# Performance work log

Hardware: AMD Instinct MI355X
Metric: run time of the kernel (lower is better)

## Reference

```python
import jax, jax.numpy as jnp
import numpy as np

HIDDEN = 2048
NUM_EXPERTS = 64
TOP_K = 8
EPS = 1e-6


def setup_inputs() -> dict:
    key = jax.random.key(0)
    k1, k2, k3, k4 = jax.random.split(key, 4)
    hidden_states = jax.random.normal(k1, (4, 4096, HIDDEN), dtype=jnp.float32)
    scale = jnp.ones((HIDDEN,), dtype=jnp.float32) + 0.01 * jax.random.normal(k2, (HIDDEN,), dtype=jnp.float32)
    proj_w = jax.random.normal(k3, (NUM_EXPERTS, HIDDEN), dtype=jnp.float32) * (HIDDEN ** -0.5)
    per_expert_scale = jnp.ones((NUM_EXPERTS,), dtype=jnp.float32) + 0.01 * jax.random.normal(k4, (NUM_EXPERTS,), dtype=jnp.float32)
    return {"hidden_states": hidden_states, "scale": scale, "proj_w": proj_w, "per_expert_scale": per_expert_scale}


def reference(hidden_states, scale, proj_w, per_expert_scale):
    H = hidden_states.shape[-1]
    # RMSNorm without learned scale
    x = hidden_states * jax.lax.rsqrt(jnp.mean(hidden_states * hidden_states, axis=-1, keepdims=True) + EPS)
    # elementwise scale and 1/sqrt(H) root-size scaling
    x = x * scale * (H ** -0.5)
    # router logits: [B,S,E]
    logits = jnp.einsum("bsh,eh->bse", x, proj_w)
    router_probs = jax.nn.softmax(logits.astype(jnp.float32), axis=-1)
    top_k_weights, top_k_index = jax.lax.top_k(router_probs, TOP_K)
    top_k_weights = top_k_weights / jnp.sum(top_k_weights, axis=-1, keepdims=True)
    top_k_weights = top_k_weights * per_expert_scale[top_k_index]
    # histc with bins=E, min=0, max=E on integer indices == bincount
    num_tokens_per_expert = jnp.bincount(top_k_index.reshape(-1), length=NUM_EXPERTS).astype(jnp.float32)
    return (top_k_weights.astype(hidden_states.dtype), top_k_index, num_tokens_per_expert)
```

## Files before the change

### kernel.cpp

```cpp
#include <hip/hip_runtime.h>
#include <math.h>

#define HIDDEN   2048
#define NEXPERT  64
#define TOPK     8
#define NTOK     16384
#define TOKB     16
#define RSQRT_H  0.02209708691207961
#define WSCALE   64.0f

typedef __attribute__((ext_vector_type(8))) _Float16       v8h;
typedef __attribute__((ext_vector_type(8))) unsigned short v8u;
typedef __attribute__((ext_vector_type(4))) float          v4f;

static __device__ __forceinline__ unsigned short f16b(float x) {
    return __builtin_bit_cast(unsigned short, (_Float16)x);
}
static __device__ __forceinline__ float f16f(unsigned short u) {
    return (float)__builtin_bit_cast(_Float16, u);
}

__global__ __launch_bounds__(256) void prep_wf(
    const float* __restrict__ w, const float* __restrict__ scale,
    unsigned short* __restrict__ wf, float* __restrict__ out_c)
{
    int i    = blockIdx.x * 256 + threadIdx.x;
    if (i < NEXPERT) out_c[i] = 0.f;
    int j    = i & 7;
    int lane = (i >> 3) & 63;
    int nt   = (i >> 9) & 3;
    int ks   = i >> 11;
    int e    = nt * 16 + (lane & 15);
    int k    = ks * 32 + (lane >> 4) * 8 + j;
    float v  = w[e * HIDDEN + k] * scale[k] * WSCALE;
    unsigned short vh = f16b(v);
    unsigned short vl = f16b(v - f16f(vh));
    size_t base = (((size_t)(ks * 4 + nt) * 2) * 64 + lane) * 8 + j;
    wf[base]       = vh;
    wf[base + 512] = vl;
}

__global__ __launch_bounds__(512, 8) void router_main(
    const float* __restrict__ h, const unsigned short* __restrict__ wf,
    const float* __restrict__ pes,
    float* __restrict__ out_w, float* __restrict__ out_i, float* __restrict__ out_c)
{
    __shared__ __align__(16) float lg[8 * 16 * 65];
    __shared__ float lss[8 * 16];
    __shared__ int   hist[NEXPERT];

    const int tid  = (int)threadIdx.x;
    const int w    = __builtin_amdgcn_readfirstlane(tid >> 6);
    const int lane = tid & 63;
    const int m    = lane & 15;
    const int quad = lane >> 4;
    const int t0   = (int)blockIdx.x * TOKB;

    if (tid < NEXPERT) hist[tid] = 0;

    const float* xp = h + (size_t)(t0 + m) * HIDDEN + w * 256 + quad * 8;
    const unsigned short* wq = wf + (size_t)(w * 8) * 4096 + (size_t)lane * 8;

    v4f acc[4];
#pragma unroll
    for (int nt = 0; nt < 4; ++nt) acc[nt] = (v4f)0.f;
    float ssl = 0.f;

    float4 xa = *(const float4*)xp;
    float4 xb = *(const float4*)(xp + 4);

    for (int i = 0; i < 8; ++i) {
        float vv[8] = {xa.x, xa.y, xa.z, xa.w, xb.x, xb.y, xb.z, xb.w};
        if (i < 7) {
            xa = *(const float4*)(xp + (i + 1) * 32);
            xb = *(const float4*)(xp + (i + 1) * 32 + 4);
        }
        v8u uh, ul;
#pragma unroll
        for (int j = 0; j < 8; ++j) {
            float v = vv[j];
            unsigned short hh = f16b(v);
            uh[j] = hh;
            ul[j] = f16b(v - f16f(hh));
            ssl   = fmaf(v, v, ssl);
        }
        v8h ah = __builtin_bit_cast(v8h, uh);
        v8h al = __builtin_bit_cast(v8h, ul);

        const unsigned short* bq = wq + (size_t)i * 4096;
#pragma unroll
        for (int nt = 0; nt < 4; ++nt) {
            const unsigned short* bp = bq + nt * 1024;
            v8h bh = *(const v8h*)bp;
            v8h bl = *(const v8h*)(bp + 512);
            acc[nt] = __builtin_amdgcn_mfma_f32_16x16x32_f16(ah, bh, acc[nt], 0, 0, 0);
            acc[nt] = __builtin_amdgcn_mfma_f32_16x16x32_f16(ah, bl, acc[nt], 0, 0, 0);
            acc[nt] = __builtin_amdgcn_mfma_f32_16x16x32_f16(al, bh, acc[nt], 0, 0, 0);
        }
    }

    {
        float s = ssl;
        s += __shfl_xor(s, 16, 64);
        s += __shfl_xor(s, 32, 64);
        if (lane < 16) lss[w * 16 + lane] = s;
    }

#pragma unroll
    for (int nt = 0; nt < 4; ++nt)
#pragma unroll
        for (int r = 0; r < 4; ++r)
            lg[(w * 16 + quad * 4 + r) * 65 + nt * 16 + m] = acc[nt][r];

    __syncthreads();

    for (int i = 0; i < 2; ++i) {
        const int tok = w * 2 + i;
        float lsum = ((lg[(0 * 16 + tok) * 65 + lane] + lg[(1 * 16 + tok) * 65 + lane])
                    + (lg[(2 * 16 + tok) * 65 + lane] + lg[(3 * 16 + tok) * 65 + lane]))
                   + ((lg[(4 * 16 + tok) * 65 + lane] + lg[(5 * 16 + tok) * 65 + lane])
                    + (lg[(6 * 16 + tok) * 65 + lane] + lg[(7 * 16 + tok) * 65 + lane]));
        float s01 = lss[0 * 16 + tok] + lss[1 * 16 + tok];
        float s23 = lss[2 * 16 + tok] + lss[3 * 16 + tok];
        float s45 = lss[4 * 16 + tok] + lss[5 * 16 + tok];
        float s67 = lss[6 * 16 + tok] + lss[7 * 16 + tok];
        double sst = (double)((s01 + s23) + (s45 + s67));
        double rr  = 1.0 / sqrt(sst * (1.0 / (double)HIDDEN) + 1e-6);
        float logit = (float)((double)lsum * rr * (RSQRT_H / (double)WSCALE));

        float work = logit;
        float myval = 0.f; int myidx = 0; float m0 = 0.f;
#pragma unroll
        for (int j = 0; j < TOPK; ++j) {
            float mx = work;
#pragma unroll
            for (int off = 32; off; off >>= 1) mx = fmaxf(mx, __shfl_xor(mx, off, 64));
            unsigned long long msk = __ballot(work == mx);
            int src = __ffsll((long long)msk) - 1;
            if (j == 0) m0 = mx;
            if (lane == j) { myval = mx; myidx = src; }
            if (lane == src) work = -3.402823466e38f;
        }

        float ev = (lane < TOPK) ? expf(myval - m0) : 0.f;
        float es = ev;
        es += __shfl_xor(es, 1, 64);
        es += __shfl_xor(es, 2, 64);
        es += __shfl_xor(es, 4, 64);
        if (lane < TOPK) {
            float wgt = (ev / es) * pes[myidx];
            size_t o = (size_t)(t0 + tok) * TOPK + lane;
            out_w[o] = wgt;
            out_i[o] = (float)myidx;
            atomicAdd(&hist[myidx], 1);
        }
    }

    __syncthreads();
    if (tid < NEXPERT)
        atomicAdd(&out_c[tid], (float)hist[tid]);
}

extern "C" void kernel_launch(void* const* d_in, const int* in_sizes, int n_in,
                              void* d_out, int out_size, void* d_ws, size_t ws_size,
                              hipStream_t stream) {
    const float* h     = (const float*)d_in[0];
    const float* scale = (const float*)d_in[1];
    const float* w     = (const float*)d_in[2];
    const float* pes   = (const float*)d_in[3];

    unsigned short* wf = (unsigned short*)d_ws;

    float* out_w = (float*)d_out;
    float* out_i = (float*)d_out + (size_t)NTOK * TOPK;
    float* out_c = (float*)d_out + (size_t)NTOK * TOPK * 2;

    prep_wf<<<512, 256, 0, stream>>>(w, scale, wf, out_c);

    router_main<<<NTOK / TOKB, 512, 0, stream>>>(h, wf, pes, out_w, out_i, out_c);
}
```

Before: 236.1 us.

## Stage hidden states via async global-to-LDS loads with double buffering and fewer warps

```diff
diff --git a/kernel.cpp b/kernel.cpp
--- a/kernel.cpp
+++ b/kernel.cpp
@@ -40,62 +40,94 @@
     wf[base + 512] = vl;
 }
 
-__global__ __launch_bounds__(512, 8) void router_main(
+__global__ __launch_bounds__(256, 4) void router_main(
     const float* __restrict__ h, const unsigned short* __restrict__ wf,
     const float* __restrict__ pes,
     float* __restrict__ out_w, float* __restrict__ out_i, float* __restrict__ out_c)
 {
-    __shared__ __align__(16) float lg[8 * 16 * 65];
-    __shared__ float lss[8 * 16];
-    __shared__ int   hist[NEXPERT];
+    __shared__ __align__(16) char smem[33280];
+    float* stage = (float*)smem;
+    float* lg    = (float*)smem;
+    float* lss   = (float*)(smem + 32768);
+    int*   hist  = (int*)(smem + 33024);
 
     const int tid  = (int)threadIdx.x;
     const int w    = __builtin_amdgcn_readfirstlane(tid >> 6);
     const int lane = tid & 63;
     const int m    = lane & 15;
     const int quad = lane >> 4;
+    const int mx7  = m & 7;
     const int t0   = (int)blockIdx.x * TOKB;
 
     if (tid < NEXPERT) hist[tid] = 0;
 
-    const float* xp = h + (size_t)(t0 + m) * HIDDEN + w * 256 + quad * 8;
-    const unsigned short* wq = wf + (size_t)(w * 8) * 4096 + (size_t)lane * 8;
+    float* const swb = stage + w * 2048;
 
     v4f acc[4];
 #pragma unroll
     for (int nt = 0; nt < 4; ++nt) acc[nt] = (v4f)0.f;
     float ssl = 0.f;
 
-    float4 xa = *(const float4*)xp;
-    float4 xb = *(const float4*)(xp + 4);
-
-    for (int i = 0; i < 8; ++i) {
-        float vv[8] = {xa.x, xa.y, xa.z, xa.w, xb.x, xb.y, xb.z, xb.w};
-        if (i < 7) {
-            xa = *(const float4*)(xp + (i + 1) * 32);
-            xb = *(const float4*)(xp + (i + 1) * 32 + 4);
-        }
-        v8u uh, ul;
-#pragma unroll
-        for (int j = 0; j < 8; ++j) {
-            float v = vv[j];
-            unsigned short hh = f16b(v);
-            uh[j] = hh;
-            ul[j] = f16b(v - f16f(hh));
-            ssl   = fmaf(v, v, ssl);
-        }
-        v8h ah = __builtin_bit_cast(v8h, uh);
-        v8h al = __builtin_bit_cast(v8h, ul);
-
-        const unsigned short* bq = wq + (size_t)i * 4096;
-#pragma unroll
-        for (int nt = 0; nt < 4; ++nt) {
-            const unsigned short* bp = bq + nt * 1024;
-            v8h bh = *(const v8h*)bp;
-            v8h bl = *(const v8h*)(bp + 512);
-            acc[nt] = __builtin_amdgcn_mfma_f32_16x16x32_f16(ah, bh, acc[nt], 0, 0, 0);
-            acc[nt] = __builtin_amdgcn_mfma_f32_16x16x32_f16(ah, bl, acc[nt], 0, 0, 0);
-            acc[nt] = __builtin_amdgcn_mfma_f32_16x16x32_f16(al, bh, acc[nt], 0, 0, 0);
+#pragma unroll
+    for (int t = 0; t < 4; ++t) {
+        int tok = t * 4 + quad;
+        const float* gp = h + (size_t)(t0 + tok) * HIDDEN + w * 512
+                        + ((m ^ (tok & 7)) << 2);
+        __builtin_amdgcn_global_load_lds(
+            (__attribute__((address_space(1))) const void*)gp,
+            (__attribute__((address_space(3))) void*)(swb + t * 256), 16, 0, 0);
+    }
+
+#pragma unroll
+    for (int c = 0; c < 8; ++c) {
+        asm volatile("s_waitcnt lgkmcnt(0)" ::: "memory");
+        if (c < 7) {
+#pragma unroll
+            for (int t = 0; t < 4; ++t) {
+                int tok = t * 4 + quad;
+                const float* gp = h + (size_t)(t0 + tok) * HIDDEN + w * 512
+                                + (c + 1) * 64 + ((m ^ (tok & 7)) << 2);
+                __builtin_amdgcn_global_load_lds(
+                    (__attribute__((address_space(1))) const void*)gp,
+                    (__attribute__((address_space(3))) void*)
+                        (swb + ((c + 1) & 1) * 1024 + t * 256), 16, 0, 0);
+            }
+            asm volatile("s_waitcnt vmcnt(4)" ::: "memory");
+        } else {
+            asm volatile("s_waitcnt vmcnt(0)" ::: "memory");
+        }
+        __builtin_amdgcn_sched_barrier(0);
+
+        const float* stg = swb + (c & 1) * 1024 + m * 64;
+#pragma unroll
+        for (int s = 0; s < 2; ++s) {
+            const int base = s * 8 + quad * 2;
+            const float4 va = *(const float4*)(stg + (((base)     ^ mx7) << 2));
+            const float4 vb = *(const float4*)(stg + (((base + 1) ^ mx7) << 2));
+            float vv[8] = {va.x, va.y, va.z, va.w, vb.x, vb.y, vb.z, vb.w};
+            v8u uh, ul;
+#pragma unroll
+            for (int j = 0; j < 8; ++j) {
+                float v = vv[j];
+                unsigned short hh = f16b(v);
+                uh[j] = hh;
+                ul[j] = f16b(v - f16f(hh));
+                ssl   = fmaf(v, v, ssl);
+            }
+            v8h ah = __builtin_bit_cast(v8h, uh);
+            v8h al = __builtin_bit_cast(v8h, ul);
+
+            const int ksg = w * 16 + c * 2 + s;
+            const unsigned short* bq = wf + (size_t)ksg * 4096 + (size_t)lane * 8;
+#pragma unroll
+            for (int nt = 0; nt < 4; ++nt) {
+                const unsigned short* bp = bq + nt * 1024;
+                v8h bh = *(const v8h*)bp;
+                v8h bl = *(const v8h*)(bp + 512);
+                acc[nt] = __builtin_amdgcn_mfma_f32_16x16x32_f16(ah, bh, acc[nt], 0, 0, 0);
+                acc[nt] = __builtin_amdgcn_mfma_f32_16x16x32_f16(ah, bl, acc[nt], 0, 0, 0);
+                acc[nt] = __builtin_amdgcn_mfma_f32_16x16x32_f16(al, bh, acc[nt], 0, 0, 0);
+            }
         }
     }
 
@@ -105,26 +137,21 @@
         s += __shfl_xor(s, 32, 64);
         if (lane < 16) lss[w * 16 + lane] = s;
     }
+    __syncthreads();
 
 #pragma unroll
     for (int nt = 0; nt < 4; ++nt)
 #pragma unroll
         for (int r = 0; r < 4; ++r)
             lg[(w * 16 + quad * 4 + r) * 65 + nt * 16 + m] = acc[nt][r];
-
     __syncthreads();
 
-    for (int i = 0; i < 2; ++i) {
-        const int tok = w * 2 + i;
-        float lsum = ((lg[(0 * 16 + tok) * 65 + lane] + lg[(1 * 16 + tok) * 65 + lane])
-                    + (lg[(2 * 16 + tok) * 65 + lane] + lg[(3 * 16 + tok) * 65 + lane]))
-                   + ((lg[(4 * 16 + tok) * 65 + lane] + lg[(5 * 16 + tok) * 65 + lane])
-                    + (lg[(6 * 16 + tok) * 65 + lane] + lg[(7 * 16 + tok) * 65 + lane]));
-        float s01 = lss[0 * 16 + tok] + lss[1 * 16 + tok];
-        float s23 = lss[2 * 16 + tok] + lss[3 * 16 + tok];
-        float s45 = lss[4 * 16 + tok] + lss[5 * 16 + tok];
-        float s67 = lss[6 * 16 + tok] + lss[7 * 16 + tok];
-        double sst = (double)((s01 + s23) + (s45 + s67));
+    for (int i = 0; i < 4; ++i) {
+        const int tok = w * 4 + i;
+        float lsum = (lg[tok * 65 + lane]        + lg[1040 + tok * 65 + lane])
+                   + (lg[2080 + tok * 65 + lane] + lg[3120 + tok * 65 + lane]);
+        float sst4 = (lss[tok] + lss[16 + tok]) + (lss[32 + tok] + lss[48 + tok]);
+        double sst = (double)sst4;
         double rr  = 1.0 / sqrt(sst * (1.0 / (double)HIDDEN) + 1e-6);
         float logit = (float)((double)lsum * rr * (RSQRT_H / (double)WSCALE));
 
@@ -177,5 +204,5 @@
 
     prep_wf<<<512, 256, 0, stream>>>(w, scale, wf, out_c);
 
-    router_main<<<NTOK / TOKB, 512, 0, stream>>>(h, wf, pes, out_w, out_i, out_c);
-}
+    router_main<<<NTOK / TOKB, 256, 0, stream>>>(h, wf, pes, out_w, out_i, out_c);
+}
```

Result: no change. 231.8 us (-1.8%).

## Process 32 tokens per block to reuse weight fragments across two MFMA tiles

Applied to the files above, without the earlier changes.

```diff
diff --git a/kernel.cpp b/kernel.cpp
--- a/kernel.cpp
+++ b/kernel.cpp
@@ -5,7 +5,7 @@
 #define NEXPERT  64
 #define TOPK     8
 #define NTOK     16384
-#define TOKB     16
+#define TOKB     32
 #define RSQRT_H  0.02209708691207961
 #define WSCALE   64.0f
 
@@ -40,13 +40,30 @@
     wf[base + 512] = vl;
 }
 
-__global__ __launch_bounds__(512, 8) void router_main(
+static __device__ __forceinline__ void cvt8(
+    float4 a, float4 b, v8h& ah, v8h& al, float& ss)
+{
+    float vv[8] = {a.x, a.y, a.z, a.w, b.x, b.y, b.z, b.w};
+    v8u uh, ul;
+#pragma unroll
+    for (int j = 0; j < 8; ++j) {
+        float v = vv[j];
+        unsigned short hh = f16b(v);
+        uh[j] = hh;
+        ul[j] = f16b(v - f16f(hh));
+        ss    = fmaf(v, v, ss);
+    }
+    ah = __builtin_bit_cast(v8h, uh);
+    al = __builtin_bit_cast(v8h, ul);
+}
+
+__global__ __launch_bounds__(512, 4) void router_main(
     const float* __restrict__ h, const unsigned short* __restrict__ wf,
     const float* __restrict__ pes,
     float* __restrict__ out_w, float* __restrict__ out_i, float* __restrict__ out_c)
 {
-    __shared__ __align__(16) float lg[8 * 16 * 65];
-    __shared__ float lss[8 * 16];
+    __shared__ __align__(16) float lg[8 * 32 * 66];
+    __shared__ float lss[8 * 32];
     __shared__ int   hist[NEXPERT];
 
     const int tid  = (int)threadIdx.x;
@@ -58,73 +75,84 @@
 
     if (tid < NEXPERT) hist[tid] = 0;
 
-    const float* xp = h + (size_t)(t0 + m) * HIDDEN + w * 256 + quad * 8;
+    const float* xp0 = h + (size_t)(t0 + m) * HIDDEN + w * 256 + quad * 8;
+    const float* xp1 = xp0 + (size_t)16 * HIDDEN;
     const unsigned short* wq = wf + (size_t)(w * 8) * 4096 + (size_t)lane * 8;
 
-    v4f acc[4];
-#pragma unroll
-    for (int nt = 0; nt < 4; ++nt) acc[nt] = (v4f)0.f;
-    float ssl = 0.f;
-
-    float4 xa = *(const float4*)xp;
-    float4 xb = *(const float4*)(xp + 4);
-
-    for (int i = 0; i < 8; ++i) {
-        float vv[8] = {xa.x, xa.y, xa.z, xa.w, xb.x, xb.y, xb.z, xb.w};
-        if (i < 7) {
-            xa = *(const float4*)(xp + (i + 1) * 32);
-            xb = *(const float4*)(xp + (i + 1) * 32 + 4);
-        }
-        v8u uh, ul;
-#pragma unroll
-        for (int j = 0; j < 8; ++j) {
-            float v = vv[j];
-            unsigned short hh = f16b(v);
-            uh[j] = hh;
-            ul[j] = f16b(v - f16f(hh));
-            ssl   = fmaf(v, v, ssl);
-        }
-        v8h ah = __builtin_bit_cast(v8h, uh);
-        v8h al = __builtin_bit_cast(v8h, ul);
-
-        const unsigned short* bq = wq + (size_t)i * 4096;
+    v4f acc0[4], acc1[4];
+#pragma unroll
+    for (int nt = 0; nt < 4; ++nt) { acc0[nt] = (v4f)0.f; acc1[nt] = (v4f)0.f; }
+    float ss0 = 0.f, ss1 = 0.f;
+
+    float4 xa0 = *(const float4*)xp0, xb0 = *(const float4*)(xp0 + 4);
+    float4 xa1 = *(const float4*)xp1, xb1 = *(const float4*)(xp1 + 4);
+
+#pragma unroll
+    for (int s = 0; s < 8; ++s) {
+        const unsigned short* bq = wq + (size_t)s * 4096;
+        v8h bh[4], bl[4];
 #pragma unroll
         for (int nt = 0; nt < 4; ++nt) {
-            const unsigned short* bp = bq + nt * 1024;
-            v8h bh = *(const v8h*)bp;
-            v8h bl = *(const v8h*)(bp + 512);
-            acc[nt] = __builtin_amdgcn_mfma_f32_16x16x32_f16(ah, bh, acc[nt], 0, 0, 0);
-            acc[nt] = __builtin_amdgcn_mfma_f32_16x16x32_f16(ah, bl, acc[nt], 0, 0, 0);
-            acc[nt] = __builtin_amdgcn_mfma_f32_16x16x32_f16(al, bh, acc[nt], 0, 0, 0);
-        }
+            bh[nt] = *(const v8h*)(bq + nt * 1024);
+            bl[nt] = *(const v8h*)(bq + nt * 1024 + 512);
+        }
+        float4 na0, nb0, na1, nb1;
+        if (s < 7) {
+            na0 = *(const float4*)(xp0 + (s + 1) * 32);
+            nb0 = *(const float4*)(xp0 + (s + 1) * 32 + 4);
+            na1 = *(const float4*)(xp1 + (s + 1) * 32);
+            nb1 = *(const float4*)(xp1 + (s + 1) * 32 + 4);
+        }
+        __builtin_amdgcn_sched_barrier(0);
+
+        v8h ah0, al0, ah1, al1;
+        cvt8(xa0, xb0, ah0, al0, ss0);
+        cvt8(xa1, xb1, ah1, al1, ss1);
+
+#pragma unroll
+        for (int nt = 0; nt < 4; ++nt) {
+            acc0[nt] = __builtin_amdgcn_mfma_f32_16x16x32_f16(ah0, bh[nt], acc0[nt], 0, 0, 0);
+            acc1[nt] = __builtin_amdgcn_mfma_f32_16x16x32_f16(ah1, bh[nt], acc1[nt], 0, 0, 0);
+            acc0[nt] = __builtin_amdgcn_mfma_f32_16x16x32_f16(ah0, bl[nt], acc0[nt], 0, 0, 0);
+            acc1[nt] = __builtin_amdgcn_mfma_f32_16x16x32_f16(ah1, bl[nt], acc1[nt], 0, 0, 0);
+            acc0[nt] = __builtin_amdgcn_mfma_f32_16x16x32_f16(al0, bh[nt], acc0[nt], 0, 0, 0);
+            acc1[nt] = __builtin_amdgcn_mfma_f32_16x16x32_f16(al1, bh[nt], acc1[nt], 0, 0, 0);
+        }
+
+        if (s < 7) { xa0 = na0; xb0 = nb0; xa1 = na1; xb1 = nb1; }
     }
 
     {
-        float s = ssl;
-        s += __shfl_xor(s, 16, 64);
-        s += __shfl_xor(s, 32, 64);
-        if (lane < 16) lss[w * 16 + lane] = s;
+        float s0 = ss0, s1 = ss1;
+        s0 += __shfl_xor(s0, 16, 64); s0 += __shfl_xor(s0, 32, 64);
+        s1 += __shfl_xor(s1, 16, 64); s1 += __shfl_xor(s1, 32, 64);
+        if (lane < 16) {
+            lss[w * 32 + lane]      = s0;
+            lss[w * 32 + 16 + lane] = s1;
+        }
     }
 
 #pragma unroll
     for (int nt = 0; nt < 4; ++nt)
 #pragma unroll
-        for (int r = 0; r < 4; ++r)
-            lg[(w * 16 + quad * 4 + r) * 65 + nt * 16 + m] = acc[nt][r];
-
+        for (int r = 0; r < 4; ++r) {
+            lg[(w * 32 + quad * 4 + r) * 66 + nt * 16 + m]      = acc0[nt][r];
+            lg[(w * 32 + 16 + quad * 4 + r) * 66 + nt * 16 + m] = acc1[nt][r];
+        }
     __syncthreads();
 
-    for (int i = 0; i < 2; ++i) {
-        const int tok = w * 2 + i;
-        float lsum = ((lg[(0 * 16 + tok) * 65 + lane] + lg[(1 * 16 + tok) * 65 + lane])
-                    + (lg[(2 * 16 + tok) * 65 + lane] + lg[(3 * 16 + tok) * 65 + lane]))
-                   + ((lg[(4 * 16 + tok) * 65 + lane] + lg[(5 * 16 + tok) * 65 + lane])
-                    + (lg[(6 * 16 + tok) * 65 + lane] + lg[(7 * 16 + tok) * 65 + lane]));
-        float s01 = lss[0 * 16 + tok] + lss[1 * 16 + tok];
-        float s23 = lss[2 * 16 + tok] + lss[3 * 16 + tok];
-        float s45 = lss[4 * 16 + tok] + lss[5 * 16 + tok];
-        float s67 = lss[6 * 16 + tok] + lss[7 * 16 + tok];
-        double sst = (double)((s01 + s23) + (s45 + s67));
+    for (int i = 0; i < 4; ++i) {
+        const int tok = w * 4 + i;
+        float l0 = lg[(0 * 32 + tok) * 66 + lane], l1 = lg[(1 * 32 + tok) * 66 + lane];
+        float l2 = lg[(2 * 32 + tok) * 66 + lane], l3 = lg[(3 * 32 + tok) * 66 + lane];
+        float l4 = lg[(4 * 32 + tok) * 66 + lane], l5 = lg[(5 * 32 + tok) * 66 + lane];
+        float l6 = lg[(6 * 32 + tok) * 66 + lane], l7 = lg[(7 * 32 + tok) * 66 + lane];
+        float lsum = ((l0 + l1) + (l2 + l3)) + ((l4 + l5) + (l6 + l7));
+        float q01 = lss[0 * 32 + tok] + lss[1 * 32 + tok];
+        float q23 = lss[2 * 32 + tok] + lss[3 * 32 + tok];
+        float q45 = lss[4 * 32 + tok] + lss[5 * 32 + tok];
+        float q67 = lss[6 * 32 + tok] + lss[7 * 32 + tok];
+        double sst = (double)((q01 + q23) + (q45 + q67));
         double rr  = 1.0 / sqrt(sst * (1.0 / (double)HIDDEN) + 1e-6);
         float logit = (float)((double)lsum * rr * (RSQRT_H / (double)WSCALE));
 
```

After: 210.3 us. 1.12x faster.

## Halve block to 4 waves with 512-wide K slices and prefetch weights ahead of MFMA

Applied to the files above, without the earlier changes.

```diff
diff --git a/kernel.cpp b/kernel.cpp
--- a/kernel.cpp
+++ b/kernel.cpp
@@ -40,13 +40,30 @@
     wf[base + 512] = vl;
 }
 
-__global__ __launch_bounds__(512, 8) void router_main(
+static __device__ __forceinline__ void cvt8(
+    float4 a, float4 b, v8h& ah, v8h& al, float& ss)
+{
+    float vv[8] = {a.x, a.y, a.z, a.w, b.x, b.y, b.z, b.w};
+    v8u uh, ul;
+#pragma unroll
+    for (int j = 0; j < 8; ++j) {
+        float v = vv[j];
+        unsigned short hh = f16b(v);
+        uh[j] = hh;
+        ul[j] = f16b(v - f16f(hh));
+        ss    = fmaf(v, v, ss);
+    }
+    ah = __builtin_bit_cast(v8h, uh);
+    al = __builtin_bit_cast(v8h, ul);
+}
+
+__global__ __launch_bounds__(256, 4) void router_main(
     const float* __restrict__ h, const unsigned short* __restrict__ wf,
     const float* __restrict__ pes,
     float* __restrict__ out_w, float* __restrict__ out_i, float* __restrict__ out_c)
 {
-    __shared__ __align__(16) float lg[8 * 16 * 65];
-    __shared__ float lss[8 * 16];
+    __shared__ __align__(16) float lg[4 * 16 * 65];
+    __shared__ float lss[4 * 16];
     __shared__ int   hist[NEXPERT];
 
     const int tid  = (int)threadIdx.x;
@@ -58,49 +75,47 @@
 
     if (tid < NEXPERT) hist[tid] = 0;
 
-    const float* xp = h + (size_t)(t0 + m) * HIDDEN + w * 256 + quad * 8;
-    const unsigned short* wq = wf + (size_t)(w * 8) * 4096 + (size_t)lane * 8;
+    const float* xp = h + (size_t)(t0 + m) * HIDDEN + w * 512 + quad * 8;
+    const unsigned short* wq = wf + (size_t)(w * 16) * 4096 + (size_t)lane * 8;
 
     v4f acc[4];
 #pragma unroll
     for (int nt = 0; nt < 4; ++nt) acc[nt] = (v4f)0.f;
-    float ssl = 0.f;
+    float ss = 0.f;
 
     float4 xa = *(const float4*)xp;
     float4 xb = *(const float4*)(xp + 4);
 
-    for (int i = 0; i < 8; ++i) {
-        float vv[8] = {xa.x, xa.y, xa.z, xa.w, xb.x, xb.y, xb.z, xb.w};
-        if (i < 7) {
-            xa = *(const float4*)(xp + (i + 1) * 32);
-            xb = *(const float4*)(xp + (i + 1) * 32 + 4);
-        }
-        v8u uh, ul;
 #pragma unroll
-        for (int j = 0; j < 8; ++j) {
-            float v = vv[j];
-            unsigned short hh = f16b(v);
-            uh[j] = hh;
-            ul[j] = f16b(v - f16f(hh));
-            ssl   = fmaf(v, v, ssl);
-        }
-        v8h ah = __builtin_bit_cast(v8h, uh);
-        v8h al = __builtin_bit_cast(v8h, ul);
-
-        const unsigned short* bq = wq + (size_t)i * 4096;
+    for (int s = 0; s < 16; ++s) {
+        const unsigned short* bq = wq + (size_t)s * 4096;
+        v8h bh[4], bl[4];
 #pragma unroll
         for (int nt = 0; nt < 4; ++nt) {
-            const unsigned short* bp = bq + nt * 1024;
-            v8h bh = *(const v8h*)bp;
-            v8h bl = *(const v8h*)(bp + 512);
-            acc[nt] = __builtin_amdgcn_mfma_f32_16x16x32_f16(ah, bh, acc[nt], 0, 0, 0);
-            acc[nt] = __builtin_amdgcn_mfma_f32_16x16x32_f16(ah, bl, acc[nt], 0, 0, 0);
-            acc[nt] = __builtin_amdgcn_mfma_f32_16x16x32_f16(al, bh, acc[nt], 0, 0, 0);
+            bh[nt] = *(const v8h*)(bq + nt * 1024);
+            bl[nt] = *(const v8h*)(bq + nt * 1024 + 512);
         }
+        float4 na, nb;
+        if (s < 15) {
+            na = *(const float4*)(xp + (s + 1) * 32);
+            nb = *(const float4*)(xp + (s + 1) * 32 + 4);
+        }
+        __builtin_amdgcn_sched_barrier(0);
+
+        v8h ah, al;
+        cvt8(xa, xb, ah, al, ss);
+#pragma unroll
+        for (int nt = 0; nt < 4; ++nt) {
+            acc[nt] = __builtin_amdgcn_mfma_f32_16x16x32_f16(ah, bh[nt], acc[nt], 0, 0, 0);
+            acc[nt] = __builtin_amdgcn_mfma_f32_16x16x32_f16(ah, bl[nt], acc[nt], 0, 0, 0);
+            acc[nt] = __builtin_amdgcn_mfma_f32_16x16x32_f16(al, bh[nt], acc[nt], 0, 0, 0);
+        }
+
+        if (s < 15) { xa = na; xb = nb; }
     }
 
     {
-        float s = ssl;
+        float s = ss;
         s += __shfl_xor(s, 16, 64);
         s += __shfl_xor(s, 32, 64);
         if (lane < 16) lss[w * 16 + lane] = s;
@@ -111,20 +126,14 @@
 #pragma unroll
         for (int r = 0; r < 4; ++r)
             lg[(w * 16 + quad * 4 + r) * 65 + nt * 16 + m] = acc[nt][r];
-
     __syncthreads();
 
-    for (int i = 0; i < 2; ++i) {
-        const int tok = w * 2 + i;
-        float lsum = ((lg[(0 * 16 + tok) * 65 + lane] + lg[(1 * 16 + tok) * 65 + lane])
-                    + (lg[(2 * 16 + tok) * 65 + lane] + lg[(3 * 16 + tok) * 65 + lane]))
-                   + ((lg[(4 * 16 + tok) * 65 + lane] + lg[(5 * 16 + tok) * 65 + lane])
-                    + (lg[(6 * 16 + tok) * 65 + lane] + lg[(7 * 16 + tok) * 65 + lane]));
-        float s01 = lss[0 * 16 + tok] + lss[1 * 16 + tok];
-        float s23 = lss[2 * 16 + tok] + lss[3 * 16 + tok];
-        float s45 = lss[4 * 16 + tok] + lss[5 * 16 + tok];
-        float s67 = lss[6 * 16 + tok] + lss[7 * 16 + tok];
-        double sst = (double)((s01 + s23) + (s45 + s67));
+    for (int i = 0; i < 4; ++i) {
+        const int tok = w * 4 + i;
+        float lsum = (lg[tok * 65 + lane]        + lg[1040 + tok * 65 + lane])
+                   + (lg[2080 + tok * 65 + lane] + lg[3120 + tok * 65 + lane]);
+        float sst4 = (lss[tok] + lss[16 + tok]) + (lss[32 + tok] + lss[48 + tok]);
+        double sst = (double)sst4;
         double rr  = 1.0 / sqrt(sst * (1.0 / (double)HIDDEN) + 1e-6);
         float logit = (float)((double)lsum * rr * (RSQRT_H / (double)WSCALE));
 
@@ -177,5 +186,5 @@
 
     prep_wf<<<512, 256, 0, stream>>>(w, scale, wf, out_c);
 
-    router_main<<<NTOK / TOKB, 512, 0, stream>>>(h, wf, pes, out_w, out_i, out_c);
+    router_main<<<NTOK / TOKB, 256, 0, stream>>>(h, wf, pes, out_w, out_i, out_c);
 }
```

Measured after the change: 226.4 us. -4.1%, faster.
